# Optimization experiments

Measured on AMD Instinct MI355X. Metric: run time of the kernel, lower is better.

The kernel has to match this reference:

```python
import jax, jax.numpy as jnp
import numpy as np

INF = 1e38  # matches torch module's INF = 1e+38


def setup_inputs() -> dict:
    key = jax.random.key(0)
    k1, k2, k3 = jax.random.split(key, 3)
    n_len, batch, dim = 2048, 4, 512
    # scale query so QK^T logits don't fully saturate the softmax
    query = jax.random.normal(k1, (n_len, batch, dim), dtype=jnp.float32) * 0.05
    W_in = jax.random.normal(k2, (dim, dim), dtype=jnp.float32) * (1.0 / np.sqrt(dim))
    W_out = jax.random.normal(k3, (dim, 2 * dim), dtype=jnp.float32) * (1.0 / np.sqrt(2 * dim))
    return {"query": query, "W_in": W_in, "W_out": W_out}


def reference(query, W_in, W_out):
    # query: [n_len, batch, dim]; torch .t() swaps first two dims -> [batch, n_len, dim]
    q = jnp.transpose(query, (1, 0, 2))
    b, n, d = q.shape
    # attention_type == 'general': linear_in (no bias), y = x @ W^T
    q = jnp.einsum('bnd,ed->bne', q, W_in)
    # scores: [b, n, n]
    scores = jnp.einsum('bnd,bmd->bnm', q, q)
    # mask = triu(ones) INCLUDING diagonal -> set to -INF (row 0 fully masked)
    mask = jnp.triu(jnp.ones((n, n), dtype=bool))
    scores = jnp.where(mask[None, :, :], -INF, scores)
    weights = jax.nn.softmax(scores, axis=-1)  # row 0 becomes uniform (all -INF)
    # manual zero-out of row 0 of the attention weights
    weights = weights.at[:, 0, :].set(0.0)
    mix = jnp.einsum('bnm,bmd->bnd', weights, q)
    combined = jnp.concatenate([mix, q], axis=-1)  # [b, n, 2d]
    out = jnp.einsum('bnk,dk->bnd', combined, W_out)  # linear_out, no bias
    out = jax.nn.selu(out)
    # final .t() -> [n_len, batch, dim]
    return jnp.transpose(out, (1, 0, 2)), weights
```

## Files before the change

### kernel.cpp

```cpp
#include <hip/hip_runtime.h>
#include <hip/hip_bf16.h>

typedef unsigned short u16;
typedef unsigned int u32;

#define BATCH 4
#define NLEN 2048
#define DIM 512
#define LDSK 40

typedef __attribute__((ext_vector_type(8))) __bf16 bf16x8;
typedef __attribute__((ext_vector_type(4))) float f32x4;

typedef const __attribute__((address_space(1))) void gv_t;
typedef __attribute__((address_space(3))) void lv_t;

__device__ __forceinline__ u16 f32_to_bf16(float f) {
  union { float f; u32 u; } v; v.f = f;
  u32 u = v.u;
  return (u16)((u + 0x7FFFu + ((u >> 16) & 1u)) >> 16);
}
__device__ __forceinline__ u32 pk2(float lo, float hi) {
  return (u32)f32_to_bf16(lo) | ((u32)f32_to_bf16(hi) << 16);
}
__device__ __forceinline__ void stage8_f32(u16* dst, const float* src) {
  float4 a = *(const float4*)src;
  float4 b = *(const float4*)(src + 4);
  uint4 o;
  o.x = pk2(a.x, a.y); o.y = pk2(a.z, a.w);
  o.z = pk2(b.x, b.y); o.w = pk2(b.z, b.w);
  *(uint4*)dst = o;
}
__device__ __forceinline__ void stage16_f32(u16* dst, const float* src) {
  stage8_f32(dst, src); stage8_f32(dst + 8, src + 8);
}
__device__ __forceinline__ u32 addpk_bf16(u32 a, u32 b) {
  float a0 = __uint_as_float(a << 16), a1 = __uint_as_float(a & 0xffff0000u);
  float b0 = __uint_as_float(b << 16), b1 = __uint_as_float(b & 0xffff0000u);
  return pk2(a0 + b0, a1 + b1);
}

template <int NRPW>
__device__ __forceinline__ void glds_rows(const u16* gsrc, size_t gstride, u16* lds,
                                          int wrow0, int lane) {
  const int r = lane >> 3;
  const int c = (lane & 7) * 8;
#pragma unroll
  for (int i = 0; i < NRPW; i += 8) {
    const int row = wrow0 + i + r;
    __builtin_amdgcn_global_load_lds((gv_t*)(gsrc + (size_t)row * gstride + c),
                                     (lv_t*)(lds + row * 64 + c), 16, 0, 0);
  }
}

__global__ __launch_bounds__(256) void k_qproj(const float* __restrict__ query,
                                               const float* __restrict__ W_in,
                                               u16* __restrict__ qp, u16* __restrict__ qt) {
  __shared__ u16 As[64 * LDSK];
  __shared__ u16 Bs[128 * LDSK];
  __shared__ u16 tbuf[128][72];
  const int t = threadIdx.x;
  const int lane = t & 63, wid = t >> 6;
  const int wm = (wid >> 1) * 32, wn = (wid & 1) * 64;
  const int lr = lane & 15, lk = (lane >> 4) * 8;
  const int trow4 = t >> 2, tseg = (t & 3) * 8;
  const int trow2 = t >> 1, thalf = (t & 1) * 16;
  const int rbase = blockIdx.y * 64;
  const int cbase = blockIdx.x * 128;
  const int rg = rbase + trow4;
  const int bb = rg >> 11, nn = rg & 2047;
  const float* aRow = query + (size_t)(nn * BATCH + bb) * DIM + tseg;
  const float* bRow = W_in + (size_t)(cbase + trow2) * DIM + thalf;
  f32x4 acc[2][4] = {};
  for (int k0 = 0; k0 < DIM; k0 += 32) {
    stage8_f32(As + trow4 * LDSK + tseg, aRow + k0);
    stage16_f32(Bs + trow2 * LDSK + thalf, bRow + k0);
    __syncthreads();
    bf16x8 af[2], bfr[4];
#pragma unroll
    for (int m = 0; m < 2; ++m) af[m] = *(const bf16x8*)(As + (wm + m * 16 + lr) * LDSK + lk);
#pragma unroll
    for (int n = 0; n < 4; ++n) bfr[n] = *(const bf16x8*)(Bs + (wn + n * 16 + lr) * LDSK + lk);
#pragma unroll
    for (int m = 0; m < 2; ++m)
#pragma unroll
      for (int n = 0; n < 4; ++n)
        acc[m][n] = __builtin_amdgcn_mfma_f32_16x16x32_bf16(af[m], bfr[n], acc[m][n], 0, 0, 0);
    __syncthreads();
  }
#pragma unroll
  for (int m = 0; m < 2; ++m)
#pragma unroll
    for (int n = 0; n < 4; ++n)
#pragma unroll
      for (int j = 0; j < 4; ++j) {
        int rl = wm + m * 16 + (lane >> 4) * 4 + j;
        int cl = wn + n * 16 + lr;
        u16 v = f32_to_bf16(acc[m][n][j]);
        qp[(size_t)(rbase + rl) * DIM + cbase + cl] = v;
        tbuf[cl][rl] = v;
      }
  __syncthreads();
  const int bb0 = rbase >> 11, nbase = rbase & 2047;
#pragma unroll
  for (int i = 0; i < 4; ++i) {
    int idx = t + i * 256;
    int dl = idx >> 3, c = idx & 7;
    uint4 v = *(const uint4*)&tbuf[dl][c * 8];
    *(uint4*)(qt + (size_t)(bb0 * DIM + cbase + dl) * NLEN + nbase + c * 8) = v;
  }
}

__global__ __launch_bounds__(256) void k_scores(const u16* __restrict__ qp,
                                                u16* __restrict__ swf) {
  const int tri = blockIdx.x;
  const int b = blockIdx.y;
  int nt = 0, cacc = 0;
  while (cacc + nt + 1 <= tri) { cacc += nt + 1; ++nt; }
  const int mt = tri - cacc;
  __shared__ u16 As[128 * 64];
  __shared__ u16 Bs[128 * 64];
  const int t = threadIdx.x;
  const int lane = t & 63, wid = t >> 6;
  const int wm = (wid >> 1) * 64, wn = (wid & 1) * 64;
  const int lr = lane & 15, lk = (lane >> 4) * 8;
  const u16* ag = qp + (size_t)(b * NLEN + nt * 128) * DIM;
  const u16* bg = qp + (size_t)(b * NLEN + mt * 128) * DIM;
  f32x4 acc[4][4] = {};
  for (int k0 = 0; k0 < DIM; k0 += 64) {
    glds_rows<32>(ag + k0, DIM, As, wid * 32, lane);
    glds_rows<32>(bg + k0, DIM, Bs, wid * 32, lane);
    __syncthreads();
#pragma unroll
    for (int kk = 0; kk < 64; kk += 32) {
      bf16x8 af[4], bfr[4];
#pragma unroll
      for (int m = 0; m < 4; ++m) af[m] = *(const bf16x8*)(As + (wm + m * 16 + lr) * 64 + kk + lk);
#pragma unroll
      for (int n = 0; n < 4; ++n) bfr[n] = *(const bf16x8*)(Bs + (wn + n * 16 + lr) * 64 + kk + lk);
#pragma unroll
      for (int m = 0; m < 4; ++m)
#pragma unroll
        for (int n = 0; n < 4; ++n)
          acc[m][n] = __builtin_amdgcn_mfma_f32_16x16x32_bf16(af[m], bfr[n], acc[m][n], 0, 0, 0);
    }
    __syncthreads();
  }
  u16* wtile = swf + ((size_t)(b * 136 + tri) << 14);
#pragma unroll
  for (int m = 0; m < 4; ++m)
#pragma unroll
    for (int n = 0; n < 4; ++n)
#pragma unroll
      for (int j = 0; j < 4; ++j) {
        int rl = wm + m * 16 + (lane >> 4) * 4 + j;
        int cl = wn + n * 16 + lr;
        wtile[rl * 128 + cl] = f32_to_bf16(acc[m][n][j]);
      }
}

__global__ __launch_bounds__(256) void k_softmax(u16* __restrict__ swf, float* __restrict__ w,
                                                 const float* __restrict__ W_out,
                                                 u16* __restrict__ wob) {
  const int n = blockIdx.x, b = blockIdx.y;
  const int t = threadIdx.x;
  if (n >= NLEN) {
    int g = ((n - NLEN) * 4 + b) * 256 + t;
#pragma unroll
    for (int i = 0; i < 4; ++i) {
      int e = g * 32 + i * 8;
      stage8_f32(wob + e, W_out + e);
    }
    return;
  }
  float* wrow = w + ((size_t)b * NLEN + n) * NLEN;
  const int nt = n >> 7;
  const size_t tb = ((size_t)(b * 136 + nt * (nt + 1) / 2) << 14) + ((size_t)(n & 127) << 7);
  __shared__ float srow[NLEN];
  __shared__ float red[4];
  if (n == 0) {
    for (int i = t; i < NLEN / 4; i += 256) ((float4*)wrow)[i] = float4{0, 0, 0, 0};
    if (t < 16) ((uint4*)(swf + tb))[t] = uint4{0, 0, 0, 0};
    return;
  }
  const int lane = t & 63, wid = t >> 6;
  const int nchunk = (nt + 1) * 16;
  float mx = -1e38f;
  for (int idx = t; idx < nchunk; idx += 256) {
    const int mt = idx >> 4, c = idx & 15;
    uint4 rv = *(const uint4*)(swf + tb + ((size_t)mt << 14) + c * 8);
    int m0 = mt * 128 + c * 8;
    u32 wds[4] = {rv.x, rv.y, rv.z, rv.w};
#pragma unroll
    for (int wi = 0; wi < 4; ++wi) {
      float v0 = __uint_as_float(wds[wi] << 16);
      float v1 = __uint_as_float(wds[wi] & 0xffff0000u);
      int m = m0 + wi * 2;
      srow[m] = v0; srow[m + 1] = v1;
      if (m < n) mx = fmaxf(mx, v0);
      if (m + 1 < n) mx = fmaxf(mx, v1);
    }
  }
#pragma unroll
  for (int off = 32; off; off >>= 1) mx = fmaxf(mx, __shfl_xor(mx, off));
  if (lane == 0) red[wid] = mx;
  __syncthreads();
  mx = fmaxf(fmaxf(red[0], red[1]), fmaxf(red[2], red[3]));
  float sum = 0.f;
  for (int m = t; m < n; m += 256) {
    float e = __expf(srow[m] - mx);
    srow[m] = e;
    sum += e;
  }
#pragma unroll
  for (int off = 32; off; off >>= 1) sum += __shfl_xor(sum, off);
  __syncthreads();
  if (lane == 0) red[wid] = sum;
  __syncthreads();
  float inv = 1.0f / (red[0] + red[1] + red[2] + red[3]);
  {
    int m0 = t * 8;
    float vals[8];
#pragma unroll
    for (int e = 0; e < 8; ++e) { int m = m0 + e; vals[e] = (m < n) ? srow[m] * inv : 0.f; }
    ((float4*)wrow)[t * 2] = float4{vals[0], vals[1], vals[2], vals[3]};
    ((float4*)wrow)[t * 2 + 1] = float4{vals[4], vals[5], vals[6], vals[7]};
  }
  for (int idx = t; idx < nchunk; idx += 256) {
    const int mt = idx >> 4, c = idx & 15;
    int m0 = mt * 128 + c * 8;
    u32 wo[4];
#pragma unroll
    for (int wi = 0; wi < 4; ++wi) {
      int m = m0 + wi * 2;
      float v0 = (m < n) ? srow[m] * inv : 0.f;
      float v1 = (m + 1 < n) ? srow[m + 1] * inv : 0.f;
      wo[wi] = (u32)f32_to_bf16(v0) | ((u32)f32_to_bf16(v1) << 16);
    }
    *(uint4*)(swf + tb + ((size_t)mt << 14) + c * 8) = uint4{wo[0], wo[1], wo[2], wo[3]};
  }
}

__global__ __launch_bounds__(256) void k_mix(const u16* __restrict__ swf,
                                             const u16* __restrict__ qt,
                                             u16* __restrict__ amix,
                                             u16* __restrict__ mix1) {
  const int j = blockIdx.x >> 4;
  const int bdt = blockIdx.x & 15;
  const int b = bdt >> 2, dt = bdt & 3;
  int nt, kt0, ktn, slot;
  if (j < 16) {
    nt = 15 - (j >> 1);
    if ((j & 1) == 0) { kt0 = 0; ktn = 8; slot = 0; }
    else { kt0 = 8; ktn = nt + 1; slot = 1; }
  } else {
    nt = 23 - j; kt0 = 0; ktn = nt + 1; slot = 0;
  }
  __shared__ u16 As[128 * 64];
  __shared__ u16 Bs[128 * 64];
  const int t = threadIdx.x;
  const int lane = t & 63, wid = t >> 6;
  const int wm = (wid >> 1) * 64, wn = (wid & 1) * 64;
  const int lr = lane & 15, lk = (lane >> 4) * 8;
  const size_t tribase = (size_t)(b * 136 + nt * (nt + 1) / 2) << 14;
  const u16* bgbase = qt + (size_t)(b * DIM + dt * 128) * NLEN;
  f32x4 acc[4][4] = {};
  for (int ks = kt0 * 2; ks < ktn * 2; ++ks) {
    const u16* ag = swf + tribase + ((size_t)(ks >> 1) << 14) + (ks & 1) * 64;
    glds_rows<32>(ag, 128, As, wid * 32, lane);
    glds_rows<32>(bgbase + ks * 64, NLEN, Bs, wid * 32, lane);
    __syncthreads();
#pragma unroll
    for (int kk = 0; kk < 64; kk += 32) {
      bf16x8 af[4], bfr[4];
#pragma unroll
      for (int m = 0; m < 4; ++m) af[m] = *(const bf16x8*)(As + (wm + m * 16 + lr) * 64 + kk + lk);
#pragma unroll
      for (int n = 0; n < 4; ++n) bfr[n] = *(const bf16x8*)(Bs + (wn + n * 16 + lr) * 64 + kk + lk);
#pragma unroll
      for (int m = 0; m < 4; ++m)
#pragma unroll
        for (int n = 0; n < 4; ++n)
          acc[m][n] = __builtin_amdgcn_mfma_f32_16x16x32_bf16(af[m], bfr[n], acc[m][n], 0, 0, 0);
    }
    __syncthreads();
  }
  u16* dst = slot ? mix1 : amix;
#pragma unroll
  for (int m = 0; m < 4; ++m)
#pragma unroll
    for (int n = 0; n < 4; ++n)
#pragma unroll
      for (int j2 = 0; j2 < 4; ++j2) {
        int row = nt * 128 + wm + m * 16 + (lane >> 4) * 4 + j2;
        int col = dt * 128 + wn + n * 16 + lr;
        dst[(size_t)(b * NLEN + row) * DIM + col] = f32_to_bf16(acc[m][n][j2]);
      }
}

__global__ __launch_bounds__(256) void k_fold(u16* __restrict__ amix,
                                              const u16* __restrict__ mix1) {
  const int t = threadIdx.x;
#pragma unroll
  for (int i = 0; i < 2; ++i) {
    int g = (blockIdx.x * 2 + i) * 256 + t;
    int rowlin = g >> 6, within = g & 63;
    int b = rowlin >> 10, n = 1024 + (rowlin & 1023);
    size_t off = ((size_t)(b * NLEN + n) * DIM) + within * 8;
    uint4 a = *(const uint4*)(amix + off);
    uint4 c = *(const uint4*)(mix1 + off);
    uint4 o;
    o.x = addpk_bf16(a.x, c.x); o.y = addpk_bf16(a.y, c.y);
    o.z = addpk_bf16(a.z, c.z); o.w = addpk_bf16(a.w, c.w);
    *(uint4*)(amix + off) = o;
  }
}

__global__ __launch_bounds__(256) void k_out(const u16* __restrict__ amix,
                                             const u16* __restrict__ qp,
                                             const u16* __restrict__ wob,
                                             float* __restrict__ out) {
  __shared__ u16 As[128 * 64];
  __shared__ u16 Bs[64 * 64];
  const int et = blockIdx.x;
  const int rt = blockIdx.y;
  const int t = threadIdx.x;
  const int lane = t & 63, wid = t >> 6;
  const int wm = (wid >> 1) * 64, wn = (wid & 1) * 32;
  const int lr = lane & 15, lk = (lane >> 4) * 8;
  const int rbase = rt * 128;
  const u16* aMix = amix + (size_t)rbase * DIM;
  const u16* aQ = qp + (size_t)rbase * DIM;
  const u16* bW = wob + (size_t)(et * 64) * (2 * DIM);
  f32x4 acc[4][2] = {};
  for (int k0 = 0; k0 < 2 * DIM; k0 += 64) {
    const u16* ag = (k0 < DIM) ? (aMix + k0) : (aQ + (k0 - DIM));
    glds_rows<32>(ag, DIM, As, wid * 32, lane);
    glds_rows<16>(bW + k0, 2 * DIM, Bs, wid * 16, lane);
    __syncthreads();
#pragma unroll
    for (int kk = 0; kk < 64; kk += 32) {
      bf16x8 af[4], bfr[2];
#pragma unroll
      for (int m = 0; m < 4; ++m) af[m] = *(const bf16x8*)(As + (wm + m * 16 + lr) * 64 + kk + lk);
#pragma unroll
      for (int n = 0; n < 2; ++n) bfr[n] = *(const bf16x8*)(Bs + (wn + n * 16 + lr) * 64 + kk + lk);
#pragma unroll
      for (int m = 0; m < 4; ++m)
#pragma unroll
        for (int n = 0; n < 2; ++n)
          acc[m][n] = __builtin_amdgcn_mfma_f32_16x16x32_bf16(af[m], bfr[n], acc[m][n], 0, 0, 0);
    }
    __syncthreads();
  }
  const float sc = 1.0507009873554805f;
  const float al = 1.6732632423543772f;
#pragma unroll
  for (int m = 0; m < 4; ++m)
#pragma unroll
    for (int n = 0; n < 2; ++n)
#pragma unroll
      for (int j = 0; j < 4; ++j) {
        int row = rbase + wm + m * 16 + (lane >> 4) * 4 + j;
        int col = et * 64 + wn + n * 16 + lr;
        int b2 = row >> 11, n2 = row & 2047;
        float v = acc[m][n][j];
        v = (v > 0.f) ? sc * v : sc * al * (__expf(v) - 1.f);
        out[(size_t)(n2 * BATCH + b2) * DIM + col] = v;
      }
}

extern "C" void kernel_launch(void* const* d_in, const int* in_sizes, int n_in,
                              void* d_out, int out_size, void* d_ws, size_t ws_size,
                              hipStream_t stream) {
  const float* query = (const float*)d_in[0];
  const float* W_in = (const float*)d_in[1];
  const float* W_out = (const float*)d_in[2];
  float* out0 = (float*)d_out;
  float* w = out0 + (size_t)NLEN * BATCH * DIM;

  const size_t PSZ = (size_t)BATCH * NLEN * DIM;
  u16* qp = (u16*)d_ws;
  u16* qt = qp + PSZ;
  u16* amix = qt + PSZ;
  u16* mix1 = amix + PSZ;
  u16* swf = mix1 + PSZ;
  u16* wob = swf + (size_t)BATCH * 136 * 16384;

  dim3 blk(256);
  k_qproj<<<dim3(DIM / 128, (BATCH * NLEN) / 64), blk, 0, stream>>>(query, W_in, qp, qt);
  k_scores<<<dim3(136, BATCH), blk, 0, stream>>>(qp, swf);
  k_softmax<<<dim3(NLEN + 16, BATCH), blk, 0, stream>>>(swf, w, W_out, wob);
  k_mix<<<dim3(384), blk, 0, stream>>>(swf, qt, amix, mix1);
  k_fold<<<dim3(512), blk, 0, stream>>>(amix, mix1);
  k_out<<<dim3(8, 64), blk, 0, stream>>>(amix, qp, wob, out0);
}
```

Baseline: 124.5 us.

## Pre-convert inputs to bf16, async-load qproj tiles, drop split-K mix fold

Adds a conversion kernel that turns query, W_in and W_out into bf16 up front. The projection GEMM can then use global_load_lds async copies with 128x64 tiles instead of converting fp32 in registers, and the W_out conversion leaves the softmax kernel. The mix kernel drops split-K plus the separate fold pass. Long rows are instead split into 64-column sub-tiles, so load is balanced without an extra add kernel or a mix1 buffer. The trade-off is an extra launch and an extra bf16 round trip of the query through memory, plus narrower tiles with less reuse for the long mix rows.

```diff
diff --git a/kernel.cpp b/kernel.cpp
--- a/kernel.cpp
+++ b/kernel.cpp
@@ -7,7 +7,6 @@
 #define BATCH 4
 #define NLEN 2048
 #define DIM 512
-#define LDSK 40
 
 typedef __attribute__((ext_vector_type(8))) __bf16 bf16x8;
 typedef __attribute__((ext_vector_type(4))) float f32x4;
@@ -23,7 +22,7 @@
 __device__ __forceinline__ u32 pk2(float lo, float hi) {
   return (u32)f32_to_bf16(lo) | ((u32)f32_to_bf16(hi) << 16);
 }
-__device__ __forceinline__ void stage8_f32(u16* dst, const float* src) {
+__device__ __forceinline__ void conv8(u16* dst, const float* src) {
   float4 a = *(const float4*)src;
   float4 b = *(const float4*)(src + 4);
   uint4 o;
@@ -31,14 +30,6 @@
   o.z = pk2(b.x, b.y); o.w = pk2(b.z, b.w);
   *(uint4*)dst = o;
 }
-__device__ __forceinline__ void stage16_f32(u16* dst, const float* src) {
-  stage8_f32(dst, src); stage8_f32(dst + 8, src + 8);
-}
-__device__ __forceinline__ u32 addpk_bf16(u32 a, u32 b) {
-  float a0 = __uint_as_float(a << 16), a1 = __uint_as_float(a & 0xffff0000u);
-  float b0 = __uint_as_float(b << 16), b1 = __uint_as_float(b & 0xffff0000u);
-  return pk2(a0 + b0, a1 + b1);
-}
 
 template <int NRPW>
 __device__ __forceinline__ void glds_rows(const u16* gsrc, size_t gstride, u16* lds,
@@ -53,45 +44,73 @@
   }
 }
 
-__global__ __launch_bounds__(256) void k_qproj(const float* __restrict__ query,
-                                               const float* __restrict__ W_in,
+__global__ __launch_bounds__(256) void k_conv(const float* __restrict__ query,
+                                              const float* __restrict__ W_in,
+                                              const float* __restrict__ W_out,
+                                              u16* __restrict__ qb, u16* __restrict__ wib,
+                                              u16* __restrict__ wob) {
+  const int NQ = BATCH * NLEN * DIM / 8;
+  const int NWI = DIM * DIM / 8;
+  const int NWO = DIM * 2 * DIM / 8;
+  const int total = NQ + NWI + NWO;
+  for (int g = blockIdx.x * 256 + threadIdx.x; g < total; g += gridDim.x * 256) {
+    if (g < NQ) conv8(qb + (size_t)g * 8, query + (size_t)g * 8);
+    else if (g < NQ + NWI) {
+      int e = g - NQ;
+      conv8(wib + (size_t)e * 8, W_in + (size_t)e * 8);
+    } else {
+      int e = g - NQ - NWI;
+      conv8(wob + (size_t)e * 8, W_out + (size_t)e * 8);
+    }
+  }
+}
+
+__global__ __launch_bounds__(256) void k_qproj(const u16* __restrict__ qb,
+                                               const u16* __restrict__ wib,
                                                u16* __restrict__ qp, u16* __restrict__ qt) {
-  __shared__ u16 As[64 * LDSK];
-  __shared__ u16 Bs[128 * LDSK];
-  __shared__ u16 tbuf[128][72];
-  const int t = threadIdx.x;
-  const int lane = t & 63, wid = t >> 6;
-  const int wm = (wid >> 1) * 32, wn = (wid & 1) * 64;
+  __shared__ u16 As[128 * 64];
+  __shared__ u16 Bs[64 * 64];
+  __shared__ u16 tbuf[64][136];
+  const int t = threadIdx.x;
+  const int lane = t & 63, wid = t >> 6;
+  const int wm = (wid >> 1) * 64, wn = (wid & 1) * 32;
   const int lr = lane & 15, lk = (lane >> 4) * 8;
-  const int trow4 = t >> 2, tseg = (t & 3) * 8;
-  const int trow2 = t >> 1, thalf = (t & 1) * 16;
-  const int rbase = blockIdx.y * 64;
-  const int cbase = blockIdx.x * 128;
-  const int rg = rbase + trow4;
-  const int bb = rg >> 11, nn = rg & 2047;
-  const float* aRow = query + (size_t)(nn * BATCH + bb) * DIM + tseg;
-  const float* bRow = W_in + (size_t)(cbase + trow2) * DIM + thalf;
-  f32x4 acc[2][4] = {};
-  for (int k0 = 0; k0 < DIM; k0 += 32) {
-    stage8_f32(As + trow4 * LDSK + tseg, aRow + k0);
-    stage16_f32(Bs + trow2 * LDSK + thalf, bRow + k0);
-    __syncthreads();
-    bf16x8 af[2], bfr[4];
-#pragma unroll
-    for (int m = 0; m < 2; ++m) af[m] = *(const bf16x8*)(As + (wm + m * 16 + lr) * LDSK + lk);
-#pragma unroll
-    for (int n = 0; n < 4; ++n) bfr[n] = *(const bf16x8*)(Bs + (wn + n * 16 + lr) * LDSK + lk);
-#pragma unroll
-    for (int m = 0; m < 2; ++m)
-#pragma unroll
-      for (int n = 0; n < 4; ++n)
-        acc[m][n] = __builtin_amdgcn_mfma_f32_16x16x32_bf16(af[m], bfr[n], acc[m][n], 0, 0, 0);
-    __syncthreads();
-  }
-#pragma unroll
-  for (int m = 0; m < 2; ++m)
-#pragma unroll
-    for (int n = 0; n < 4; ++n)
+  const int et = blockIdx.x;
+  const int rt = blockIdx.y;
+  const int rbase = rt * 128, cbase = et * 64;
+  const int b0 = rbase >> 11, nbase = rbase & 2047;
+  const int ar = lane >> 3, ac = (lane & 7) * 8;
+  f32x4 acc[4][2] = {};
+  for (int k0 = 0; k0 < DIM; k0 += 64) {
+#pragma unroll
+    for (int i = 0; i < 32; i += 8) {
+      const int row = wid * 32 + i + ar;
+      const int nn = nbase + row;
+      __builtin_amdgcn_global_load_lds(
+          (gv_t*)(qb + (size_t)(nn * BATCH + b0) * DIM + k0 + ac),
+          (lv_t*)(As + row * 64 + ac), 16, 0, 0);
+    }
+    glds_rows<16>(wib + (size_t)cbase * DIM + k0, DIM, Bs, wid * 16, lane);
+    __syncthreads();
+#pragma unroll
+    for (int kk = 0; kk < 64; kk += 32) {
+      bf16x8 af[4], bfr[2];
+#pragma unroll
+      for (int m = 0; m < 4; ++m) af[m] = *(const bf16x8*)(As + (wm + m * 16 + lr) * 64 + kk + lk);
+#pragma unroll
+      for (int n = 0; n < 2; ++n) bfr[n] = *(const bf16x8*)(Bs + (wn + n * 16 + lr) * 64 + kk + lk);
+#pragma unroll
+      for (int m = 0; m < 4; ++m)
+#pragma unroll
+        for (int n = 0; n < 2; ++n)
+          acc[m][n] = __builtin_amdgcn_mfma_f32_16x16x32_bf16(af[m], bfr[n], acc[m][n], 0, 0, 0);
+    }
+    __syncthreads();
+  }
+#pragma unroll
+  for (int m = 0; m < 4; ++m)
+#pragma unroll
+    for (int n = 0; n < 2; ++n)
 #pragma unroll
       for (int j = 0; j < 4; ++j) {
         int rl = wm + m * 16 + (lane >> 4) * 4 + j;
@@ -101,13 +120,12 @@
         tbuf[cl][rl] = v;
       }
   __syncthreads();
-  const int bb0 = rbase >> 11, nbase = rbase & 2047;
 #pragma unroll
   for (int i = 0; i < 4; ++i) {
     int idx = t + i * 256;
-    int dl = idx >> 3, c = idx & 7;
+    int dl = idx >> 4, c = idx & 15;
     uint4 v = *(const uint4*)&tbuf[dl][c * 8];
-    *(uint4*)(qt + (size_t)(bb0 * DIM + cbase + dl) * NLEN + nbase + c * 8) = v;
+    *(uint4*)(qt + (size_t)(b0 * DIM + cbase + dl) * NLEN + nbase + c * 8) = v;
   }
 }
 
@@ -159,20 +177,9 @@
       }
 }
 
-__global__ __launch_bounds__(256) void k_softmax(u16* __restrict__ swf, float* __restrict__ w,
-                                                 const float* __restrict__ W_out,
-                                                 u16* __restrict__ wob) {
+__global__ __launch_bounds__(256) void k_softmax(u16* __restrict__ swf, float* __restrict__ w) {
   const int n = blockIdx.x, b = blockIdx.y;
   const int t = threadIdx.x;
-  if (n >= NLEN) {
-    int g = ((n - NLEN) * 4 + b) * 256 + t;
-#pragma unroll
-    for (int i = 0; i < 4; ++i) {
-      int e = g * 32 + i * 8;
-      stage8_f32(wob + e, W_out + e);
-    }
-    return;
-  }
   float* wrow = w + ((size_t)b * NLEN + n) * NLEN;
   const int nt = n >> 7;
   const size_t tb = ((size_t)(b * 136 + nt * (nt + 1) / 2) << 14) + ((size_t)(n & 127) << 7);
@@ -241,78 +248,69 @@
   }
 }
 
+template <int NCOLS>
+__device__ __forceinline__ void mix_body(u16* As, u16* Bs,
+                                         const u16* __restrict__ swf,
+                                         const u16* __restrict__ qt,
+                                         u16* __restrict__ amix,
+                                         int b, int nt, int sub) {
+  constexpr int NR = NCOLS / 32;
+  const int t = threadIdx.x;
+  const int lane = t & 63, wid = t >> 6;
+  const int wm = (wid >> 1) * 64, wn = (wid & 1) * (NCOLS / 2);
+  const int lr = lane & 15, lk = (lane >> 4) * 8;
+  const size_t tribase = (size_t)(b * 136 + nt * (nt + 1) / 2) << 14;
+  const u16* bgbase = qt + (size_t)(b * DIM + sub * NCOLS) * NLEN;
+  f32x4 acc[4][NR] = {};
+  const int nks = (nt + 1) * 2;
+  for (int ks = 0; ks < nks; ++ks) {
+    const u16* ag = swf + tribase + ((size_t)(ks >> 1) << 14) + (ks & 1) * 64;
+    glds_rows<32>(ag, 128, As, wid * 32, lane);
+    if (NCOLS == 128) glds_rows<32>(bgbase + ks * 64, NLEN, Bs, wid * 32, lane);
+    else glds_rows<16>(bgbase + ks * 64, NLEN, Bs, wid * 16, lane);
+    __syncthreads();
+#pragma unroll
+    for (int kk = 0; kk < 64; kk += 32) {
+      bf16x8 af[4], bfr[NR];
+#pragma unroll
+      for (int m = 0; m < 4; ++m) af[m] = *(const bf16x8*)(As + (wm + m * 16 + lr) * 64 + kk + lk);
+#pragma unroll
+      for (int n = 0; n < NR; ++n) bfr[n] = *(const bf16x8*)(Bs + (wn + n * 16 + lr) * 64 + kk + lk);
+#pragma unroll
+      for (int m = 0; m < 4; ++m)
+#pragma unroll
+        for (int n = 0; n < NR; ++n)
+          acc[m][n] = __builtin_amdgcn_mfma_f32_16x16x32_bf16(af[m], bfr[n], acc[m][n], 0, 0, 0);
+    }
+    __syncthreads();
+  }
+#pragma unroll
+  for (int m = 0; m < 4; ++m)
+#pragma unroll
+    for (int n = 0; n < NR; ++n)
+#pragma unroll
+      for (int j2 = 0; j2 < 4; ++j2) {
+        int row = nt * 128 + wm + m * 16 + (lane >> 4) * 4 + j2;
+        int col = sub * NCOLS + wn + n * 16 + lr;
+        amix[(size_t)(b * NLEN + row) * DIM + col] = f32_to_bf16(acc[m][n][j2]);
+      }
+}
+
 __global__ __launch_bounds__(256) void k_mix(const u16* __restrict__ swf,
                                              const u16* __restrict__ qt,
-                                             u16* __restrict__ amix,
-                                             u16* __restrict__ mix1) {
-  const int j = blockIdx.x >> 4;
-  const int bdt = blockIdx.x & 15;
-  const int b = bdt >> 2, dt = bdt & 3;
-  int nt, kt0, ktn, slot;
-  if (j < 16) {
-    nt = 15 - (j >> 1);
-    if ((j & 1) == 0) { kt0 = 0; ktn = 8; slot = 0; }
-    else { kt0 = 8; ktn = nt + 1; slot = 1; }
-  } else {
-    nt = 23 - j; kt0 = 0; ktn = nt + 1; slot = 0;
-  }
+                                             u16* __restrict__ amix) {
   __shared__ u16 As[128 * 64];
   __shared__ u16 Bs[128 * 64];
-  const int t = threadIdx.x;
-  const int lane = t & 63, wid = t >> 6;
-  const int wm = (wid >> 1) * 64, wn = (wid & 1) * 64;
-  const int lr = lane & 15, lk = (lane >> 4) * 8;
-  const size_t tribase = (size_t)(b * 136 + nt * (nt + 1) / 2) << 14;
-  const u16* bgbase = qt + (size_t)(b * DIM + dt * 128) * NLEN;
-  f32x4 acc[4][4] = {};
-  for (int ks = kt0 * 2; ks < ktn * 2; ++ks) {
-    const u16* ag = swf + tribase + ((size_t)(ks >> 1) << 14) + (ks & 1) * 64;
-    glds_rows<32>(ag, 128, As, wid * 32, lane);
-    glds_rows<32>(bgbase + ks * 64, NLEN, Bs, wid * 32, lane);
-    __syncthreads();
-#pragma unroll
-    for (int kk = 0; kk < 64; kk += 32) {
-      bf16x8 af[4], bfr[4];
-#pragma unroll
-      for (int m = 0; m < 4; ++m) af[m] = *(const bf16x8*)(As + (wm + m * 16 + lr) * 64 + kk + lk);
-#pragma unroll
-      for (int n = 0; n < 4; ++n) bfr[n] = *(const bf16x8*)(Bs + (wn + n * 16 + lr) * 64 + kk + lk);
-#pragma unroll
-      for (int m = 0; m < 4; ++m)
-#pragma unroll
-        for (int n = 0; n < 4; ++n)
-          acc[m][n] = __builtin_amdgcn_mfma_f32_16x16x32_bf16(af[m], bfr[n], acc[m][n], 0, 0, 0);
-    }
-    __syncthreads();
-  }
-  u16* dst = slot ? mix1 : amix;
-#pragma unroll
-  for (int m = 0; m < 4; ++m)
-#pragma unroll
-    for (int n = 0; n < 4; ++n)
-#pragma unroll
-      for (int j2 = 0; j2 < 4; ++j2) {
-        int row = nt * 128 + wm + m * 16 + (lane >> 4) * 4 + j2;
-        int col = dt * 128 + wn + n * 16 + lr;
-        dst[(size_t)(b * NLEN + row) * DIM + col] = f32_to_bf16(acc[m][n][j2]);
-      }
-}
-
-__global__ __launch_bounds__(256) void k_fold(u16* __restrict__ amix,
-                                              const u16* __restrict__ mix1) {
-  const int t = threadIdx.x;
-#pragma unroll
-  for (int i = 0; i < 2; ++i) {
-    int g = (blockIdx.x * 2 + i) * 256 + t;
-    int rowlin = g >> 6, within = g & 63;
-    int b = rowlin >> 10, n = 1024 + (rowlin & 1023);
-    size_t off = ((size_t)(b * NLEN + n) * DIM) + within * 8;
-    uint4 a = *(const uint4*)(amix + off);
-    uint4 c = *(const uint4*)(mix1 + off);
-    uint4 o;
-    o.x = addpk_bf16(a.x, c.x); o.y = addpk_bf16(a.y, c.y);
-    o.z = addpk_bf16(a.z, c.z); o.w = addpk_bf16(a.w, c.w);
-    *(uint4*)(amix + off) = o;
+  const int bid = blockIdx.x;
+  if (bid < 256) {
+    const int j = bid >> 2, b = bid & 3;
+    const int nt = 15 - (j >> 3), sub = j & 7;
+    mix_body<64>(As, Bs, swf, qt, amix, b, nt, sub);
+  } else {
+    const int r = bid - 256;
+    const int j = r >> 2, b = r & 3;
+    const int nt = 7 - (j >> 2), sub = j & 3;
+    mix_body<128>(As, Bs, swf, qt, amix, b, nt, sub);
   }
 }
 
@@ -383,15 +381,16 @@
   u16* qp = (u16*)d_ws;
   u16* qt = qp + PSZ;
   u16* amix = qt + PSZ;
-  u16* mix1 = amix + PSZ;
-  u16* swf = mix1 + PSZ;
-  u16* wob = swf + (size_t)BATCH * 136 * 16384;
+  u16* qb = amix + PSZ;
+  u16* swf = qb + PSZ;
+  u16* wib = swf + (size_t)BATCH * 136 * 16384;
+  u16* wob = wib + (size_t)DIM * DIM;
 
   dim3 blk(256);
-  k_qproj<<<dim3(DIM / 128, (BATCH * NLEN) / 64), blk, 0, stream>>>(query, W_in, qp, qt);
+  k_conv<<<dim3(1024), blk, 0, stream>>>(query, W_in, W_out, qb, wib, wob);
+  k_qproj<<<dim3(8, 64), blk, 0, stream>>>(qb, wib, qp, qt);
   k_scores<<<dim3(136, BATCH), blk, 0, stream>>>(qp, swf);
-  k_softmax<<<dim3(NLEN + 16, BATCH), blk, 0, stream>>>(swf, w, W_out, wob);
-  k_mix<<<dim3(384), blk, 0, stream>>>(swf, qt, amix, mix1);
-  k_fold<<<dim3(512), blk, 0, stream>>>(amix, mix1);
+  k_softmax<<<dim3(NLEN, BATCH), blk, 0, stream>>>(swf, w);
+  k_mix<<<dim3(384), blk, 0, stream>>>(swf, qt, amix);
   k_out<<<dim3(8, 64), blk, 0, stream>>>(amix, qp, wob, out0);
 }
```

Result: slower. 127.9 us (+2.7%).

## Fuse exp and row-sum into scores kernel, defer normalization to mix

Applied to the files above, without the earlier changes.

The scores kernel now applies the causal mask, computes exp without max subtraction, writes the unnormalized exponentials, and emits per-tile partial row sums. The softmax kernel becomes a light normalization pass that sums the partials, writes the fp32 weights, and stores a per-row inverse, which the mix kernel applies to its accumulators before output. This removes the separate max and sum passes and the bf16 rewrite of the score tiles. It relies on the logits being small enough that exp does not overflow without a max shift, and it also remaps the k_out grid to a swizzled 1D order for better locality.

```diff
diff --git a/kernel.cpp b/kernel.cpp
--- a/kernel.cpp
+++ b/kernel.cpp
@@ -112,7 +112,8 @@
 }
 
 __global__ __launch_bounds__(256) void k_scores(const u16* __restrict__ qp,
-                                                u16* __restrict__ swf) {
+                                                u16* __restrict__ swf,
+                                                float* __restrict__ spart) {
   const int tri = blockIdx.x;
   const int b = blockIdx.y;
   int nt = 0, cacc = 0;
@@ -120,6 +121,7 @@
   const int mt = tri - cacc;
   __shared__ u16 As[128 * 64];
   __shared__ u16 Bs[128 * 64];
+  __shared__ float ssum[128][2];
   const int t = threadIdx.x;
   const int lane = t & 63, wid = t >> 6;
   const int wm = (wid >> 1) * 64, wn = (wid & 1) * 64;
@@ -147,6 +149,11 @@
     __syncthreads();
   }
   u16* wtile = swf + ((size_t)(b * 136 + tri) << 14);
+  float rs[4][4];
+#pragma unroll
+  for (int m = 0; m < 4; ++m)
+#pragma unroll
+    for (int j = 0; j < 4; ++j) rs[m][j] = 0.f;
 #pragma unroll
   for (int m = 0; m < 4; ++m)
 #pragma unroll
@@ -155,13 +162,32 @@
       for (int j = 0; j < 4; ++j) {
         int rl = wm + m * 16 + (lane >> 4) * 4 + j;
         int cl = wn + n * 16 + lr;
-        wtile[rl * 128 + cl] = f32_to_bf16(acc[m][n][j]);
+        bool valid = (mt * 128 + cl) < (nt * 128 + rl);
+        float e = valid ? __expf(acc[m][n][j]) : 0.f;
+        wtile[rl * 128 + cl] = f32_to_bf16(e);
+        rs[m][j] += e;
       }
-}
-
-__global__ __launch_bounds__(256) void k_softmax(u16* __restrict__ swf, float* __restrict__ w,
-                                                 const float* __restrict__ W_out,
-                                                 u16* __restrict__ wob) {
+#pragma unroll
+  for (int m = 0; m < 4; ++m)
+#pragma unroll
+    for (int j = 0; j < 4; ++j) {
+      float v = rs[m][j];
+      v += __shfl_xor(v, 1);
+      v += __shfl_xor(v, 2);
+      v += __shfl_xor(v, 4);
+      v += __shfl_xor(v, 8);
+      if ((lane & 15) == 0) ssum[wm + m * 16 + (lane >> 4) * 4 + j][wid & 1] = v;
+    }
+  __syncthreads();
+  if (t < 128) spart[(size_t)(b * 136 + tri) * 128 + t] = ssum[t][0] + ssum[t][1];
+}
+
+__global__ __launch_bounds__(256) void k_wnorm(const u16* __restrict__ swf,
+                                               const float* __restrict__ spart,
+                                               float* __restrict__ w,
+                                               float* __restrict__ rowinv,
+                                               const float* __restrict__ W_out,
+                                               u16* __restrict__ wob) {
   const int n = blockIdx.x, b = blockIdx.y;
   const int t = threadIdx.x;
   if (n >= NLEN) {
@@ -173,76 +199,36 @@
     }
     return;
   }
+  const int nt = n >> 7;
+  const int tri0 = nt * (nt + 1) / 2;
+  float s = 0.f;
+  for (int mt = 0; mt <= nt; ++mt)
+    s += spart[(size_t)(b * 136 + tri0 + mt) * 128 + (n & 127)];
+  const float inv = (n == 0) ? 0.f : 1.0f / s;
+  if (t == 0) rowinv[b * NLEN + n] = inv;
   float* wrow = w + ((size_t)b * NLEN + n) * NLEN;
-  const int nt = n >> 7;
-  const size_t tb = ((size_t)(b * 136 + nt * (nt + 1) / 2) << 14) + ((size_t)(n & 127) << 7);
-  __shared__ float srow[NLEN];
-  __shared__ float red[4];
-  if (n == 0) {
-    for (int i = t; i < NLEN / 4; i += 256) ((float4*)wrow)[i] = float4{0, 0, 0, 0};
-    if (t < 16) ((uint4*)(swf + tb))[t] = uint4{0, 0, 0, 0};
-    return;
-  }
-  const int lane = t & 63, wid = t >> 6;
-  const int nchunk = (nt + 1) * 16;
-  float mx = -1e38f;
-  for (int idx = t; idx < nchunk; idx += 256) {
-    const int mt = idx >> 4, c = idx & 15;
-    uint4 rv = *(const uint4*)(swf + tb + ((size_t)mt << 14) + c * 8);
-    int m0 = mt * 128 + c * 8;
-    u32 wds[4] = {rv.x, rv.y, rv.z, rv.w};
-#pragma unroll
-    for (int wi = 0; wi < 4; ++wi) {
-      float v0 = __uint_as_float(wds[wi] << 16);
-      float v1 = __uint_as_float(wds[wi] & 0xffff0000u);
-      int m = m0 + wi * 2;
-      srow[m] = v0; srow[m + 1] = v1;
-      if (m < n) mx = fmaxf(mx, v0);
-      if (m + 1 < n) mx = fmaxf(mx, v1);
-    }
-  }
-#pragma unroll
-  for (int off = 32; off; off >>= 1) mx = fmaxf(mx, __shfl_xor(mx, off));
-  if (lane == 0) red[wid] = mx;
-  __syncthreads();
-  mx = fmaxf(fmaxf(red[0], red[1]), fmaxf(red[2], red[3]));
-  float sum = 0.f;
-  for (int m = t; m < n; m += 256) {
-    float e = __expf(srow[m] - mx);
-    srow[m] = e;
-    sum += e;
-  }
-#pragma unroll
-  for (int off = 32; off; off >>= 1) sum += __shfl_xor(sum, off);
-  __syncthreads();
-  if (lane == 0) red[wid] = sum;
-  __syncthreads();
-  float inv = 1.0f / (red[0] + red[1] + red[2] + red[3]);
-  {
-    int m0 = t * 8;
-    float vals[8];
-#pragma unroll
-    for (int e = 0; e < 8; ++e) { int m = m0 + e; vals[e] = (m < n) ? srow[m] * inv : 0.f; }
-    ((float4*)wrow)[t * 2] = float4{vals[0], vals[1], vals[2], vals[3]};
-    ((float4*)wrow)[t * 2 + 1] = float4{vals[4], vals[5], vals[6], vals[7]};
-  }
-  for (int idx = t; idx < nchunk; idx += 256) {
-    const int mt = idx >> 4, c = idx & 15;
-    int m0 = mt * 128 + c * 8;
-    u32 wo[4];
-#pragma unroll
-    for (int wi = 0; wi < 4; ++wi) {
-      int m = m0 + wi * 2;
-      float v0 = (m < n) ? srow[m] * inv : 0.f;
-      float v1 = (m + 1 < n) ? srow[m + 1] * inv : 0.f;
-      wo[wi] = (u32)f32_to_bf16(v0) | ((u32)f32_to_bf16(v1) << 16);
-    }
-    *(uint4*)(swf + tb + ((size_t)mt << 14) + c * 8) = uint4{wo[0], wo[1], wo[2], wo[3]};
-  }
+  const int c8 = t * 8;
+  float4 o0 = {0, 0, 0, 0}, o1 = {0, 0, 0, 0};
+  if (c8 < (nt + 1) * 128) {
+    const int mt = c8 >> 7;
+    uint4 rv = *(const uint4*)(swf + ((size_t)(b * 136 + tri0 + mt) << 14) +
+                               ((size_t)(n & 127) << 7) + (c8 & 127));
+    o0.x = __uint_as_float(rv.x << 16) * inv;
+    o0.y = __uint_as_float(rv.x & 0xffff0000u) * inv;
+    o0.z = __uint_as_float(rv.y << 16) * inv;
+    o0.w = __uint_as_float(rv.y & 0xffff0000u) * inv;
+    o1.x = __uint_as_float(rv.z << 16) * inv;
+    o1.y = __uint_as_float(rv.z & 0xffff0000u) * inv;
+    o1.z = __uint_as_float(rv.w << 16) * inv;
+    o1.w = __uint_as_float(rv.w & 0xffff0000u) * inv;
+  }
+  ((float4*)wrow)[t * 2] = o0;
+  ((float4*)wrow)[t * 2 + 1] = o1;
 }
 
 __global__ __launch_bounds__(256) void k_mix(const u16* __restrict__ swf,
                                              const u16* __restrict__ qt,
+                                             const float* __restrict__ rowinv,
                                              u16* __restrict__ amix,
                                              u16* __restrict__ mix1) {
   const int j = blockIdx.x >> 4;
@@ -289,13 +275,15 @@
 #pragma unroll
   for (int m = 0; m < 4; ++m)
 #pragma unroll
-    for (int n = 0; n < 4; ++n)
-#pragma unroll
-      for (int j2 = 0; j2 < 4; ++j2) {
-        int row = nt * 128 + wm + m * 16 + (lane >> 4) * 4 + j2;
+    for (int j2 = 0; j2 < 4; ++j2) {
+      int row = nt * 128 + wm + m * 16 + (lane >> 4) * 4 + j2;
+      float inv = rowinv[b * NLEN + row];
+#pragma unroll
+      for (int n = 0; n < 4; ++n) {
         int col = dt * 128 + wn + n * 16 + lr;
-        dst[(size_t)(b * NLEN + row) * DIM + col] = f32_to_bf16(acc[m][n][j2]);
+        dst[(size_t)(b * NLEN + row) * DIM + col] = f32_to_bf16(acc[m][n][j2] * inv);
       }
+    }
 }
 
 __global__ __launch_bounds__(256) void k_fold(u16* __restrict__ amix,
@@ -322,8 +310,9 @@
                                              float* __restrict__ out) {
   __shared__ u16 As[128 * 64];
   __shared__ u16 Bs[64 * 64];
-  const int et = blockIdx.x;
-  const int rt = blockIdx.y;
+  const int bid = blockIdx.x;
+  const int et = (bid >> 3) & 7;
+  const int rt = ((bid >> 6) << 3) | (bid & 7);
   const int t = threadIdx.x;
   const int lane = t & 63, wid = t >> 6;
   const int wm = (wid >> 1) * 64, wn = (wid & 1) * 32;
@@ -386,12 +375,14 @@
   u16* mix1 = amix + PSZ;
   u16* swf = mix1 + PSZ;
   u16* wob = swf + (size_t)BATCH * 136 * 16384;
+  float* spart = (float*)(wob + (size_t)DIM * 2 * DIM);
+  float* rowinv = spart + (size_t)BATCH * 136 * 128;
 
   dim3 blk(256);
   k_qproj<<<dim3(DIM / 128, (BATCH * NLEN) / 64), blk, 0, stream>>>(query, W_in, qp, qt);
-  k_scores<<<dim3(136, BATCH), blk, 0, stream>>>(qp, swf);
-  k_softmax<<<dim3(NLEN + 16, BATCH), blk, 0, stream>>>(swf, w, W_out, wob);
-  k_mix<<<dim3(384), blk, 0, stream>>>(swf, qt, amix, mix1);
+  k_scores<<<dim3(136, BATCH), blk, 0, stream>>>(qp, swf, spart);
+  k_wnorm<<<dim3(NLEN + 16, BATCH), blk, 0, stream>>>(swf, spart, w, rowinv, W_out, wob);
+  k_mix<<<dim3(384), blk, 0, stream>>>(swf, qt, rowinv, amix, mix1);
   k_fold<<<dim3(512), blk, 0, stream>>>(amix, mix1);
-  k_out<<<dim3(8, 64), blk, 0, stream>>>(amix, qp, wob, out0);
-}
+  k_out<<<dim3(512), blk, 0, stream>>>(amix, qp, wob, out0);
+}
```

Measured after the change: 127.2 us. +2.2%, slower.

## Reassociate output projection: precompute q·W_out halves, fuse SELU into mix epilogue

Applied to the files above, without the earlier changes.

Uses associativity: out = selu(P·(q·W1ᵀ) + q·W2ᵀ). A new k_z GEMM computes z1 = q·W1ᵀ (stored transposed) and y2 = q·W2ᵀ up front, so the attention-mix GEMM consumes z1 directly. The mix epilogue adds y2 and applies SELU, writing final output for rows that need no split-K fold. Split rows go through a small k_final kernel, which replaces the separate fold and output GEMM kernels and their intermediate traffic. Total GEMM FLOPs stay about the same, but one kernel launch and several full-size bf16 round trips are removed. The change adds bf16 rounding of z1 before the weight multiply.

```diff
diff --git a/kernel.cpp b/kernel.cpp
--- a/kernel.cpp
+++ b/kernel.cpp
@@ -19,6 +19,9 @@
   union { float f; u32 u; } v; v.f = f;
   u32 u = v.u;
   return (u16)((u + 0x7FFFu + ((u >> 16) & 1u)) >> 16);
+}
+__device__ __forceinline__ float bf16_to_f32(u16 h) {
+  return __uint_as_float(((u32)h) << 16);
 }
 __device__ __forceinline__ u32 pk2(float lo, float hi) {
   return (u32)f32_to_bf16(lo) | ((u32)f32_to_bf16(hi) << 16);
@@ -34,10 +37,10 @@
 __device__ __forceinline__ void stage16_f32(u16* dst, const float* src) {
   stage8_f32(dst, src); stage8_f32(dst + 8, src + 8);
 }
-__device__ __forceinline__ u32 addpk_bf16(u32 a, u32 b) {
-  float a0 = __uint_as_float(a << 16), a1 = __uint_as_float(a & 0xffff0000u);
-  float b0 = __uint_as_float(b << 16), b1 = __uint_as_float(b & 0xffff0000u);
-  return pk2(a0 + b0, a1 + b1);
+__device__ __forceinline__ float selu(float v) {
+  const float sc = 1.0507009873554805f;
+  const float al = 1.6732632423543772f;
+  return (v > 0.f) ? sc * v : sc * al * (__expf(v) - 1.f);
 }
 
 template <int NRPW>
@@ -53,12 +56,19 @@
   }
 }
 
+__global__ __launch_bounds__(256) void k_conv(const float* __restrict__ W_out,
+                                              u16* __restrict__ wob) {
+  int g = blockIdx.x * 1024 + threadIdx.x;
+#pragma unroll
+  for (int i = 0; i < 4; ++i, g += 256)
+    stage8_f32(wob + (size_t)g * 8, W_out + (size_t)g * 8);
+}
+
 __global__ __launch_bounds__(256) void k_qproj(const float* __restrict__ query,
                                                const float* __restrict__ W_in,
-                                               u16* __restrict__ qp, u16* __restrict__ qt) {
+                                               u16* __restrict__ qp) {
   __shared__ u16 As[64 * LDSK];
   __shared__ u16 Bs[128 * LDSK];
-  __shared__ u16 tbuf[128][72];
   const int t = threadIdx.x;
   const int lane = t & 63, wid = t >> 6;
   const int wm = (wid >> 1) * 32, wn = (wid & 1) * 64;
@@ -96,18 +106,77 @@
       for (int j = 0; j < 4; ++j) {
         int rl = wm + m * 16 + (lane >> 4) * 4 + j;
         int cl = wn + n * 16 + lr;
-        u16 v = f32_to_bf16(acc[m][n][j]);
-        qp[(size_t)(rbase + rl) * DIM + cbase + cl] = v;
-        tbuf[cl][rl] = v;
+        qp[(size_t)(rbase + rl) * DIM + cbase + cl] = f32_to_bf16(acc[m][n][j]);
       }
-  __syncthreads();
-  const int bb0 = rbase >> 11, nbase = rbase & 2047;
-#pragma unroll
-  for (int i = 0; i < 4; ++i) {
-    int idx = t + i * 256;
-    int dl = idx >> 3, c = idx & 7;
-    uint4 v = *(const uint4*)&tbuf[dl][c * 8];
-    *(uint4*)(qt + (size_t)(bb0 * DIM + cbase + dl) * NLEN + nbase + c * 8) = v;
+}
+
+__global__ __launch_bounds__(256) void k_z(const u16* __restrict__ qp,
+                                           const u16* __restrict__ wob,
+                                           u16* __restrict__ z1t, u16* __restrict__ y2) {
+  __shared__ u16 As[128 * 64];
+  __shared__ u16 Bs[128 * 64];
+  __shared__ u16 tbuf[128][136];
+  const int vt = blockIdx.x;
+  const int rt = blockIdx.y;
+  const int t = threadIdx.x;
+  const int lane = t & 63, wid = t >> 6;
+  const int wm = (wid >> 1) * 64, wn = (wid & 1) * 64;
+  const int lr = lane & 15, lk = (lane >> 4) * 8;
+  const int rbase = rt * 128, vbase = vt * 128;
+  const u16* ag = qp + (size_t)rbase * DIM;
+  const u16* bg = (vt < 4) ? (wob + (size_t)vbase * 1024)
+                           : (wob + (size_t)(vbase - 512) * 1024 + 512);
+  f32x4 acc[4][4] = {};
+  for (int k0 = 0; k0 < DIM; k0 += 64) {
+    glds_rows<32>(ag + k0, DIM, As, wid * 32, lane);
+    glds_rows<32>(bg + k0, 1024, Bs, wid * 32, lane);
+    __syncthreads();
+#pragma unroll
+    for (int kk = 0; kk < 64; kk += 32) {
+      bf16x8 af[4], bfr[4];
+#pragma unroll
+      for (int m = 0; m < 4; ++m) af[m] = *(const bf16x8*)(As + (wm + m * 16 + lr) * 64 + kk + lk);
+#pragma unroll
+      for (int n = 0; n < 4; ++n) bfr[n] = *(const bf16x8*)(Bs + (wn + n * 16 + lr) * 64 + kk + lk);
+#pragma unroll
+      for (int m = 0; m < 4; ++m)
+#pragma unroll
+        for (int n = 0; n < 4; ++n)
+          acc[m][n] = __builtin_amdgcn_mfma_f32_16x16x32_bf16(af[m], bfr[n], acc[m][n], 0, 0, 0);
+    }
+    __syncthreads();
+  }
+  if (vt < 4) {
+#pragma unroll
+    for (int m = 0; m < 4; ++m)
+#pragma unroll
+      for (int n = 0; n < 4; ++n)
+#pragma unroll
+        for (int j = 0; j < 4; ++j) {
+          int rl = wm + m * 16 + (lane >> 4) * 4 + j;
+          int cl = wn + n * 16 + lr;
+          tbuf[cl][rl] = f32_to_bf16(acc[m][n][j]);
+        }
+    __syncthreads();
+    const int b0 = rbase >> 11, nbase = rbase & 2047;
+#pragma unroll
+    for (int i = 0; i < 8; ++i) {
+      int idx = t + i * 256;
+      int dl = idx >> 4, c = idx & 15;
+      uint4 v = *(const uint4*)&tbuf[dl][c * 8];
+      *(uint4*)(z1t + (size_t)(b0 * DIM + vbase + dl) * NLEN + nbase + c * 8) = v;
+    }
+  } else {
+#pragma unroll
+    for (int m = 0; m < 4; ++m)
+#pragma unroll
+      for (int n = 0; n < 4; ++n)
+#pragma unroll
+        for (int j = 0; j < 4; ++j) {
+          int rl = wm + m * 16 + (lane >> 4) * 4 + j;
+          int cl = wn + n * 16 + lr;
+          y2[(size_t)(rbase + rl) * DIM + (vbase - 512) + cl] = f32_to_bf16(acc[m][n][j]);
+        }
   }
 }
 
@@ -159,20 +228,9 @@
       }
 }
 
-__global__ __launch_bounds__(256) void k_softmax(u16* __restrict__ swf, float* __restrict__ w,
-                                                 const float* __restrict__ W_out,
-                                                 u16* __restrict__ wob) {
+__global__ __launch_bounds__(256) void k_softmax(u16* __restrict__ swf, float* __restrict__ w) {
   const int n = blockIdx.x, b = blockIdx.y;
   const int t = threadIdx.x;
-  if (n >= NLEN) {
-    int g = ((n - NLEN) * 4 + b) * 256 + t;
-#pragma unroll
-    for (int i = 0; i < 4; ++i) {
-      int e = g * 32 + i * 8;
-      stage8_f32(wob + e, W_out + e);
-    }
-    return;
-  }
   float* wrow = w + ((size_t)b * NLEN + n) * NLEN;
   const int nt = n >> 7;
   const size_t tb = ((size_t)(b * 136 + nt * (nt + 1) / 2) << 14) + ((size_t)(n & 127) << 7);
@@ -241,10 +299,12 @@
   }
 }
 
-__global__ __launch_bounds__(256) void k_mix(const u16* __restrict__ swf,
-                                             const u16* __restrict__ qt,
-                                             u16* __restrict__ amix,
-                                             u16* __restrict__ mix1) {
+__global__ __launch_bounds__(256) void k_mixw(const u16* __restrict__ swf,
+                                              const u16* __restrict__ z1t,
+                                              const u16* __restrict__ y2,
+                                              u16* __restrict__ mixw0,
+                                              u16* __restrict__ mixw1,
+                                              float* __restrict__ out) {
   const int j = blockIdx.x >> 4;
   const int bdt = blockIdx.x & 15;
   const int b = bdt >> 2, dt = bdt & 3;
@@ -263,7 +323,7 @@
   const int wm = (wid >> 1) * 64, wn = (wid & 1) * 64;
   const int lr = lane & 15, lk = (lane >> 4) * 8;
   const size_t tribase = (size_t)(b * 136 + nt * (nt + 1) / 2) << 14;
-  const u16* bgbase = qt + (size_t)(b * DIM + dt * 128) * NLEN;
+  const u16* bgbase = z1t + (size_t)(b * DIM + dt * 128) * NLEN;
   f32x4 acc[4][4] = {};
   for (int ks = kt0 * 2; ks < ktn * 2; ++ks) {
     const u16* ag = swf + tribase + ((size_t)(ks >> 1) << 14) + (ks & 1) * 64;
@@ -285,89 +345,66 @@
     }
     __syncthreads();
   }
-  u16* dst = slot ? mix1 : amix;
-#pragma unroll
-  for (int m = 0; m < 4; ++m)
-#pragma unroll
-    for (int n = 0; n < 4; ++n)
+  if (slot == 0) {
+#pragma unroll
+    for (int m = 0; m < 4; ++m)
 #pragma unroll
       for (int j2 = 0; j2 < 4; ++j2) {
         int row = nt * 128 + wm + m * 16 + (lane >> 4) * 4 + j2;
-        int col = dt * 128 + wn + n * 16 + lr;
-        dst[(size_t)(b * NLEN + row) * DIM + col] = f32_to_bf16(acc[m][n][j2]);
+#pragma unroll
+        for (int n = 0; n < 4; ++n) {
+          int col = dt * 128 + wn + n * 16 + lr;
+          float v = acc[m][n][j2] +
+                    bf16_to_f32(y2[(size_t)(b * NLEN + row) * DIM + col]);
+          if (nt < 8) {
+            out[(size_t)(row * BATCH + b) * DIM + col] = selu(v);
+          } else {
+            mixw0[(size_t)(b * 1024 + row - 1024) * DIM + col] = f32_to_bf16(v);
+          }
+        }
       }
-}
-
-__global__ __launch_bounds__(256) void k_fold(u16* __restrict__ amix,
-                                              const u16* __restrict__ mix1) {
-  const int t = threadIdx.x;
-#pragma unroll
-  for (int i = 0; i < 2; ++i) {
-    int g = (blockIdx.x * 2 + i) * 256 + t;
-    int rowlin = g >> 6, within = g & 63;
-    int b = rowlin >> 10, n = 1024 + (rowlin & 1023);
-    size_t off = ((size_t)(b * NLEN + n) * DIM) + within * 8;
-    uint4 a = *(const uint4*)(amix + off);
-    uint4 c = *(const uint4*)(mix1 + off);
-    uint4 o;
-    o.x = addpk_bf16(a.x, c.x); o.y = addpk_bf16(a.y, c.y);
-    o.z = addpk_bf16(a.z, c.z); o.w = addpk_bf16(a.w, c.w);
-    *(uint4*)(amix + off) = o;
-  }
-}
-
-__global__ __launch_bounds__(256) void k_out(const u16* __restrict__ amix,
-                                             const u16* __restrict__ qp,
-                                             const u16* __restrict__ wob,
-                                             float* __restrict__ out) {
-  __shared__ u16 As[128 * 64];
-  __shared__ u16 Bs[64 * 64];
-  const int et = blockIdx.x;
-  const int rt = blockIdx.y;
-  const int t = threadIdx.x;
-  const int lane = t & 63, wid = t >> 6;
-  const int wm = (wid >> 1) * 64, wn = (wid & 1) * 32;
-  const int lr = lane & 15, lk = (lane >> 4) * 8;
-  const int rbase = rt * 128;
-  const u16* aMix = amix + (size_t)rbase * DIM;
-  const u16* aQ = qp + (size_t)rbase * DIM;
-  const u16* bW = wob + (size_t)(et * 64) * (2 * DIM);
-  f32x4 acc[4][2] = {};
-  for (int k0 = 0; k0 < 2 * DIM; k0 += 64) {
-    const u16* ag = (k0 < DIM) ? (aMix + k0) : (aQ + (k0 - DIM));
-    glds_rows<32>(ag, DIM, As, wid * 32, lane);
-    glds_rows<16>(bW + k0, 2 * DIM, Bs, wid * 16, lane);
-    __syncthreads();
-#pragma unroll
-    for (int kk = 0; kk < 64; kk += 32) {
-      bf16x8 af[4], bfr[2];
-#pragma unroll
-      for (int m = 0; m < 4; ++m) af[m] = *(const bf16x8*)(As + (wm + m * 16 + lr) * 64 + kk + lk);
-#pragma unroll
-      for (int n = 0; n < 2; ++n) bfr[n] = *(const bf16x8*)(Bs + (wn + n * 16 + lr) * 64 + kk + lk);
-#pragma unroll
-      for (int m = 0; m < 4; ++m)
-#pragma unroll
-        for (int n = 0; n < 2; ++n)
-          acc[m][n] = __builtin_amdgcn_mfma_f32_16x16x32_bf16(af[m], bfr[n], acc[m][n], 0, 0, 0);
-    }
-    __syncthreads();
-  }
-  const float sc = 1.0507009873554805f;
-  const float al = 1.6732632423543772f;
-#pragma unroll
-  for (int m = 0; m < 4; ++m)
-#pragma unroll
-    for (int n = 0; n < 2; ++n)
-#pragma unroll
-      for (int j = 0; j < 4; ++j) {
-        int row = rbase + wm + m * 16 + (lane >> 4) * 4 + j;
-        int col = et * 64 + wn + n * 16 + lr;
-        int b2 = row >> 11, n2 = row & 2047;
-        float v = acc[m][n][j];
-        v = (v > 0.f) ? sc * v : sc * al * (__expf(v) - 1.f);
-        out[(size_t)(n2 * BATCH + b2) * DIM + col] = v;
+  } else {
+#pragma unroll
+    for (int m = 0; m < 4; ++m)
+#pragma unroll
+      for (int j2 = 0; j2 < 4; ++j2) {
+        int row = nt * 128 + wm + m * 16 + (lane >> 4) * 4 + j2;
+#pragma unroll
+        for (int n = 0; n < 4; ++n) {
+          int col = dt * 128 + wn + n * 16 + lr;
+          mixw1[(size_t)(b * 1024 + row - 1024) * DIM + col] = f32_to_bf16(acc[m][n][j2]);
+        }
       }
+  }
+}
+
+__global__ __launch_bounds__(256) void k_final(const u16* __restrict__ mixw0,
+                                               const u16* __restrict__ mixw1,
+                                               float* __restrict__ out) {
+  const int g = blockIdx.x * 256 + threadIdx.x;
+  const int rowlin = g >> 5, ch = g & 31;
+  const int b = rowlin >> 10, n = 1024 + (rowlin & 1023);
+  const size_t moff = (size_t)rowlin * DIM + ch * 16;
+  float* orow = out + (size_t)(n * BATCH + b) * DIM + ch * 16;
+#pragma unroll
+  for (int h = 0; h < 2; ++h) {
+    uint4 a = *(const uint4*)(mixw0 + moff + h * 8);
+    uint4 c = *(const uint4*)(mixw1 + moff + h * 8);
+    u32 wa[4] = {a.x, a.y, a.z, a.w};
+    u32 wc[4] = {c.x, c.y, c.z, c.w};
+    float4 o0, o1;
+    float* op = (float*)&o0;
+#pragma unroll
+    for (int i = 0; i < 4; ++i) {
+      float lo = __uint_as_float(wa[i] << 16) + __uint_as_float(wc[i] << 16);
+      float hi = __uint_as_float(wa[i] & 0xffff0000u) + __uint_as_float(wc[i] & 0xffff0000u);
+      if (i < 2) { ((float*)&o0)[i * 2] = selu(lo); ((float*)&o0)[i * 2 + 1] = selu(hi); }
+      else { ((float*)&o1)[(i - 2) * 2] = selu(lo); ((float*)&o1)[(i - 2) * 2 + 1] = selu(hi); }
+    }
+    (void)op;
+    *(float4*)(orow + h * 8) = o0;
+    *(float4*)(orow + h * 8 + 4) = o1;
+  }
 }
 
 extern "C" void kernel_launch(void* const* d_in, const int* in_sizes, int n_in,
@@ -381,17 +418,19 @@
 
   const size_t PSZ = (size_t)BATCH * NLEN * DIM;
   u16* qp = (u16*)d_ws;
-  u16* qt = qp + PSZ;
-  u16* amix = qt + PSZ;
-  u16* mix1 = amix + PSZ;
-  u16* swf = mix1 + PSZ;
+  u16* z1t = qp + PSZ;
+  u16* y2 = z1t + PSZ;
+  u16* mixw0 = y2 + PSZ;
+  u16* mixw1 = mixw0 + PSZ / 2;
+  u16* swf = mixw1 + PSZ / 2;
   u16* wob = swf + (size_t)BATCH * 136 * 16384;
 
   dim3 blk(256);
-  k_qproj<<<dim3(DIM / 128, (BATCH * NLEN) / 64), blk, 0, stream>>>(query, W_in, qp, qt);
+  k_conv<<<dim3(64), blk, 0, stream>>>(W_out, wob);
+  k_qproj<<<dim3(DIM / 128, (BATCH * NLEN) / 64), blk, 0, stream>>>(query, W_in, qp);
+  k_z<<<dim3(8, 64), blk, 0, stream>>>(qp, wob, z1t, y2);
   k_scores<<<dim3(136, BATCH), blk, 0, stream>>>(qp, swf);
-  k_softmax<<<dim3(NLEN + 16, BATCH), blk, 0, stream>>>(swf, w, W_out, wob);
-  k_mix<<<dim3(384), blk, 0, stream>>>(swf, qt, amix, mix1);
-  k_fold<<<dim3(512), blk, 0, stream>>>(amix, mix1);
-  k_out<<<dim3(8, 64), blk, 0, stream>>>(amix, qp, wob, out0);
-}
+  k_softmax<<<dim3(NLEN, BATCH), blk, 0, stream>>>(swf, w);
+  k_mixw<<<dim3(384), blk, 0, stream>>>(swf, z1t, y2, mixw0, mixw1, out0);
+  k_final<<<dim3(512), blk, 0, stream>>>(mixw0, mixw1, out0);
+}
```

Result: slower. 140.1 us (+12.5%).
